# Kernel tuning notes

Hardware: AMD Instinct MI355X
Metric: run time of the kernel (lower is better)

## Reference

```python
import jax, jax.numpy as jnp
import numpy as np

B, N, E, H = 4, 2048, 512, 8
D = E // H  # head dim = 64


def setup_inputs() -> dict:
    key = jax.random.key(0)
    ks = jax.random.split(key, 5)
    s = 1.0 / np.sqrt(E)
    return {
        "x": jax.random.normal(ks[0], (B, N, E), dtype=jnp.float32),
        "Wk": jax.random.normal(ks[1], (E, E), dtype=jnp.float32) * s,
        "bk": jax.random.normal(ks[2], (E,), dtype=jnp.float32) * s,
        "Wv": jax.random.normal(ks[3], (E, E), dtype=jnp.float32) * s,
        "bv": jax.random.normal(ks[4], (E,), dtype=jnp.float32) * s,
    }


def reference(x, Wk, bk, Wv, bv):
    b, n, e = x.shape
    # Linear projections (torch Linear: y = x @ W.T + b), split into heads.
    keys = (x @ Wk.T + bk).reshape(b, n, H, D).transpose(0, 2, 1, 3)    # b h n d
    values = (x @ Wv.T + bv).reshape(b, n, H, D).transpose(0, 2, 1, 3)  # b h n d
    # Q = K self-attention: scores [b, h, n, n]
    dotprod = jnp.einsum('bhnd,bhmd->bhnm', keys, keys)
    # softmax over last axis, then unusual POST-softmax scaling by sqrt(emb)
    att = jax.nn.softmax(dotprod, axis=-1) / jnp.sqrt(jnp.asarray(e, x.dtype))
    # dropout p=0 -> identity
    out = jnp.einsum('bhnm,bhmd->bhnd', att, values)
    return out.transpose(0, 2, 1, 3).reshape(b, n, e)
```

## Files before the change

kernel.cpp:

```cpp
#include <hip/hip_runtime.h>

typedef __bf16 bf16_t;
typedef bf16_t bf16x8 __attribute__((ext_vector_type(8)));
typedef float f32x4 __attribute__((ext_vector_type(4)));
typedef short s16x4 __attribute__((ext_vector_type(4)));

#define NSEQ 2048
#define EMB 512
#define HEADS 8
#define HD 64
#define BATCH 4
#define LOG2E 1.4426950408889634f

#define MFMA16(a, b, c) __builtin_amdgcn_mfma_f32_16x16x32_bf16(a, b, c, 0, 0, 0)
#define MFMA1K(a, b, c) __builtin_amdgcn_mfma_f32_16x16x16bf16_1k(a, b, c, 0, 0, 0)


__global__ __launch_bounds__(256, 2) void proj_kernel(
    const float* __restrict__ x,
    const float* __restrict__ Wk, const float* __restrict__ bk,
    const float* __restrict__ Wv, const float* __restrict__ bv,
    bf16_t* __restrict__ Kf, bf16_t* __restrict__ Vf)
{
  __shared__ union {
    struct {
      __align__(16) bf16_t A[2][128][40];
      __align__(16) bf16_t B[2][128][40];
    } s;
    __align__(16) bf16_t T[128][136];
  } u;

  const int t    = threadIdx.x;
  const int w    = t >> 6;
  const int lane = t & 63;
  const int quad = lane >> 4;
  const int l15  = lane & 15;
  const int wr   = w >> 1, wc = w & 1;
  const int m0   = blockIdx.x * 128;
  const int n0   = blockIdx.y * 128;
  const int zz   = (blockIdx.y >= 4);
  const float* __restrict__ W = zz ? Wv : Wk;
  const int nW = n0 - zz * 512;

  const int sr = t >> 3;
  const int sj = t & 7;
  const int sb = sj >> 2, sc = (sj & 3) * 8;

  float4 pa[4][2], pb[4][2];
  auto prefetch = [&](int k0) {
#pragma unroll
    for (int i = 0; i < 4; ++i) {
      const float* xa = x + (size_t)(m0 + sr + i * 32) * EMB + k0 + sj * 8;
      const float* wa = W + (size_t)(nW + sr + i * 32) * EMB + k0 + sj * 8;
      pa[i][0] = *(const float4*)xa; pa[i][1] = *(const float4*)(xa + 4);
      pb[i][0] = *(const float4*)wa; pb[i][1] = *(const float4*)(wa + 4);
    }
  };
  auto pack8 = [](float4 a, float4 b) -> bf16x8 {
    bf16x8 v;
    v[0] = (bf16_t)a.x; v[1] = (bf16_t)a.y; v[2] = (bf16_t)a.z; v[3] = (bf16_t)a.w;
    v[4] = (bf16_t)b.x; v[5] = (bf16_t)b.y; v[6] = (bf16_t)b.z; v[7] = (bf16_t)b.w;
    return v;
  };

  f32x4 acc[4][4] = {};
  prefetch(0);

  for (int it = 0; it < 8; ++it) {
    __syncthreads();
#pragma unroll
    for (int i = 0; i < 4; ++i) {
      *(bf16x8*)(&u.s.A[sb][sr + i * 32][sc]) = pack8(pa[i][0], pa[i][1]);
      *(bf16x8*)(&u.s.B[sb][sr + i * 32][sc]) = pack8(pb[i][0], pb[i][1]);
    }
    __syncthreads();
    if (it < 7) prefetch((it + 1) * 64);

    bf16x8 af[4][2], bf[4][2];
#pragma unroll
    for (int mt = 0; mt < 4; ++mt)
#pragma unroll
      for (int kk = 0; kk < 2; ++kk)
        af[mt][kk] = *(const bf16x8*)(&u.s.A[kk][wr * 64 + mt * 16 + l15][quad * 8]);
#pragma unroll
    for (int nt = 0; nt < 4; ++nt)
#pragma unroll
      for (int kk = 0; kk < 2; ++kk)
        bf[nt][kk] = *(const bf16x8*)(&u.s.B[kk][wc * 64 + nt * 16 + l15][quad * 8]);
#pragma unroll
    for (int kk = 0; kk < 2; ++kk)
#pragma unroll
      for (int mt = 0; mt < 4; ++mt)
#pragma unroll
        for (int nt = 0; nt < 4; ++nt)
          acc[mt][nt] = MFMA16(af[mt][kk], bf[nt][kk], acc[mt][nt]);
  }

  __syncthreads();

#pragma unroll
  for (int mt = 0; mt < 4; ++mt) {
#pragma unroll
    for (int nt = 0; nt < 4; ++nt) {
      const int F = wc * 64 + nt * 16 + l15;
      const int c = n0 + F;
      const float bb = zz ? bv[c - 512] : bk[c];
#pragma unroll
      for (int reg = 0; reg < 4; ++reg) {
        const int R = wr * 64 + mt * 16 + quad * 4 + reg;
        const float v = acc[mt][nt][reg] + bb;
        if (!zz) u.T[R][F] = (bf16_t)v;
        else     u.T[F][R] = (bf16_t)v;
      }
    }
  }
  __syncthreads();

  if (!zz) {
#pragma unroll
    for (int i = 0; i < 8; ++i) {
      const int fi  = i * 4 + w;
      const int hL  = fi >> 4, kk = (fi >> 3) & 1, ktl = fi & 7;
      const bf16x8 v = *(const bf16x8*)(&u.T[ktl * 16 + l15][hL * 64 + kk * 32 + quad * 8]);
      const int gr = m0 + ktl * 16 + l15;
      const int b = gr >> 11, n = gr & (NSEQ - 1);
      const int bh = b * HEADS + (n0 >> 6) + hL;
      bf16_t* dst = Kf + (((size_t)(bh * 128 + (n >> 4)) * 2 + kk)) * 512 + lane * 8;
      *(bf16x8*)dst = v;
    }
  } else {
#pragma unroll
    for (int i = 0; i < 8; ++i) {
      const int fi   = i * 4 + w;
      const int hL   = fi >> 4, dt = (fi >> 2) & 3, k32l = fi & 3;
      const int F = hL * 64 + dt * 16 + l15;
      union { bf16_t h[8]; bf16x8 v; } pk2;
#pragma unroll
      for (int jt = 0; jt < 2; ++jt)
        *(uint2*)(&pk2.h[jt * 4]) =
            *(const uint2*)(&u.T[F][k32l * 32 + jt * 16 + quad * 4]);
      const int gr = m0 + k32l * 32;
      const int b = gr >> 11, n = gr & (NSEQ - 1);
      const int bh = b * HEADS + ((n0 - 512) >> 6) + hL;
      bf16_t* dst = Vf + (((size_t)(bh * 64 + (n >> 5)) * 4 + dt)) * 512 + lane * 8;
      *(bf16x8*)dst = pk2.v;
    }
  }
}

__global__ __launch_bounds__(256, 2) void flash_kernel(
    const bf16_t* __restrict__ Kf, const bf16_t* __restrict__ Vf,
    float* __restrict__ out)
{
  __shared__ struct {
    __align__(16) float Cb[2][4096];
    __align__(16) float Lb[2][64][4];
  } u;

  const int t    = threadIdx.x;
  const int w    = t >> 6;
  const int lane = t & 63;
  const int quad = lane >> 4;
  const int l15  = lane & 15;
  const int rh   = w & 1;
  const int kh   = w >> 1;

  const int bh = blockIdx.x;
  const int b  = bh >> 3, h = bh & 7;
  const int rowbase = blockIdx.y * 128 + rh * 64;
  const int qtile   = rowbase >> 4;

  const bf16_t* __restrict__ Kb = Kf + (size_t)bh * 128 * 2 * 512;
  const bf16_t* __restrict__ Vb = Vf + (size_t)bh * 64 * 4 * 512;

  bf16x8 qf[4][2];
#pragma unroll
  for (int nt = 0; nt < 4; ++nt)
#pragma unroll
    for (int kk = 0; kk < 2; ++kk)
      qf[nt][kk] = *(const bf16x8*)(Kb + ((size_t)(qtile + nt) * 2 + kk) * 512 + lane * 8);

  float mlog[4];
#pragma unroll
  for (int nt = 0; nt < 4; ++nt) {
    float ss = 0.f;
#pragma unroll
    for (int kk = 0; kk < 2; ++kk)
#pragma unroll
      for (int j = 0; j < 8; ++j) {
        const float qv = (float)qf[nt][kk][j];
        ss = fmaf(qv, qv, ss);
      }
    ss += __shfl_xor(ss, 16, 64);
    ss += __shfl_xor(ss, 32, 64);
    mlog[nt] = ss * LOG2E;
  }

  f32x4 accot[4][4] = {};
  float lsum[4] = {0.f, 0.f, 0.f, 0.f};

  auto load_k = [&](int kt, bf16x8 (&dst)[2][2]) {
    const int kb = kt * 4 + kh * 2;
#pragma unroll
    for (int jt = 0; jt < 2; ++jt)
#pragma unroll
      for (int kk = 0; kk < 2; ++kk)
        dst[jt][kk] =
            *(const bf16x8*)(Kb + ((size_t)(kb + jt) * 2 + kk) * 512 + lane * 8);
  };

  auto body = [&](int kt, bf16x8 (&kcur)[2][2], bf16x8 (&knxt)[2][2]) {
    union { bf16x8 v8; s16x4 s4[2]; } vf[4];
    const int v32 = kt * 2 + kh;
#pragma unroll
    for (int dt = 0; dt < 4; ++dt)
      vf[dt].v8 = *(const bf16x8*)(Vb + ((size_t)v32 * 4 + dt) * 512 + lane * 8);

    f32x4 st[2][4] = {};
#pragma unroll
    for (int kk = 0; kk < 2; ++kk)
#pragma unroll
      for (int jt = 0; jt < 2; ++jt)
#pragma unroll
        for (int nt = 0; nt < 4; ++nt)
          st[jt][nt] = MFMA16(kcur[jt][kk], qf[nt][kk], st[jt][nt]);

    load_k(kt + 1 < NSEQ / 64 ? kt + 1 : kt, knxt);

    s16x4 pw[2][4];
#pragma unroll
    for (int jt = 0; jt < 2; ++jt)
#pragma unroll
      for (int nt = 0; nt < 4; ++nt) {
        union { bf16_t h[4]; s16x4 s; } pp;
#pragma unroll
        for (int reg = 0; reg < 4; ++reg) {
          const float p =
              __builtin_amdgcn_exp2f(fmaf(st[jt][nt][reg], LOG2E, -mlog[nt]));
          lsum[nt] += p;
          pp.h[reg] = (bf16_t)p;
        }
        pw[jt][nt] = pp.s;
      }

#pragma unroll
    for (int jt = 0; jt < 2; ++jt)
#pragma unroll
      for (int dt = 0; dt < 4; ++dt)
#pragma unroll
        for (int nt = 0; nt < 4; ++nt)
          accot[dt][nt] = MFMA1K(vf[dt].s4[jt], pw[jt][nt], accot[dt][nt]);
  };

  bf16x8 kA[2][2], kB[2][2];
  load_k(0, kA);
  for (int kt = 0; kt < NSEQ / 64; kt += 2) {
    body(kt,     kA, kB);
    body(kt + 1, kB, kA);
  }

  __syncthreads();
  if (kh == 1) {
#pragma unroll
    for (int dt = 0; dt < 4; ++dt)
#pragma unroll
      for (int nt = 0; nt < 4; ++nt)
        *(f32x4*)(&u.Cb[rh][((dt * 4 + nt) * 64 + lane) * 4]) = accot[dt][nt];
#pragma unroll
    for (int nt = 0; nt < 4; ++nt) u.Lb[rh][lane][nt] = lsum[nt];
  }
  __syncthreads();
  if (kh == 0) {
#pragma unroll
    for (int dt = 0; dt < 4; ++dt)
#pragma unroll
      for (int nt = 0; nt < 4; ++nt)
        accot[dt][nt] += *(const f32x4*)(&u.Cb[rh][((dt * 4 + nt) * 64 + lane) * 4]);

    const float SCL = 0.044194173824159216f;
    float f[4];
#pragma unroll
    for (int nt = 0; nt < 4; ++nt) {
      float l = lsum[nt] + u.Lb[rh][lane][nt];
      l += __shfl_xor(l, 16, 64);
      l += __shfl_xor(l, 32, 64);
      f[nt] = SCL / l;
    }

#pragma unroll
    for (int nt = 0; nt < 4; ++nt) {
      const int n = rowbase + nt * 16 + l15;
      float* op = out + ((size_t)(b * NSEQ + n)) * EMB + h * HD;
#pragma unroll
      for (int dt = 0; dt < 4; ++dt) {
        f32x4 v = accot[dt][nt];
#pragma unroll
        for (int reg = 0; reg < 4; ++reg) v[reg] *= f[nt];
        *(f32x4*)(op + dt * 16 + quad * 4) = v;
      }
    }
  }
}

extern "C" void kernel_launch(void* const* d_in, const int* in_sizes, int n_in,
                              void* d_out, int out_size, void* d_ws, size_t ws_size,
                              hipStream_t stream) {
  const float* x  = (const float*)d_in[0];
  const float* Wk = (const float*)d_in[1];
  const float* bk = (const float*)d_in[2];
  const float* Wv = (const float*)d_in[3];
  const float* bv = (const float*)d_in[4];
  float* out = (float*)d_out;

  bf16_t* Kf = (bf16_t*)d_ws;
  bf16_t* Vf = Kf + (size_t)BATCH * HEADS * NSEQ * HD;

  dim3 pg(8192 / 128, 1024 / 128);
  proj_kernel<<<pg, 256, 0, stream>>>(x, Wk, bk, Wv, bv, Kf, Vf);

  dim3 fg(BATCH * HEADS, NSEQ / 128);
  flash_kernel<<<fg, 256, 0, stream>>>(Kf, Vf, out);
}
```

Measured before the change: 132.9 us.

## Split key sequence four ways per block and halve query rows per block

Each flash block now handles 64 query rows, and its four waves each take a quarter of the key range, where before two row halves each split keys two ways. The grid doubles to 1024 blocks and launch bounds rise to four blocks per SM, aiming for more parallelism and better latency hiding on the many-CU GPU. In exchange, each K/V tile is reused by fewer query rows, so global/L2 traffic rises, and the final reduction now takes a two-stage LDS tree with extra barriers. The tighter launch bound may also force register spills.

New measurement: 399.7 us. 201% more time.

```diff
diff --git a/kernel.cpp b/kernel.cpp
--- a/kernel.cpp
+++ b/kernel.cpp
@@ -148,7 +148,7 @@
   }
 }
 
-__global__ __launch_bounds__(256, 2) void flash_kernel(
+__global__ __launch_bounds__(256, 4) void flash_kernel(
     const bf16_t* __restrict__ Kf, const bf16_t* __restrict__ Vf,
     float* __restrict__ out)
 {
@@ -162,12 +162,11 @@
   const int lane = t & 63;
   const int quad = lane >> 4;
   const int l15  = lane & 15;
-  const int rh   = w & 1;
-  const int kh   = w >> 1;
+  const int kh   = w;
 
   const int bh = blockIdx.x;
   const int b  = bh >> 3, h = bh & 7;
-  const int rowbase = blockIdx.y * 128 + rh * 64;
+  const int rowbase = blockIdx.y * 64;
   const int qtile   = rowbase >> 4;
 
   const bf16_t* __restrict__ Kb = Kf + (size_t)bh * 128 * 2 * 512;
@@ -200,7 +199,7 @@
   float lsum[4] = {0.f, 0.f, 0.f, 0.f};
 
   auto load_k = [&](int kt, bf16x8 (&dst)[2][2]) {
-    const int kb = kt * 4 + kh * 2;
+    const int kb = kt * 8 + kh * 2;
 #pragma unroll
     for (int jt = 0; jt < 2; ++jt)
 #pragma unroll
@@ -211,7 +210,7 @@
 
   auto body = [&](int kt, bf16x8 (&kcur)[2][2], bf16x8 (&knxt)[2][2]) {
     union { bf16x8 v8; s16x4 s4[2]; } vf[4];
-    const int v32 = kt * 2 + kh;
+    const int v32 = kt * 4 + kh;
 #pragma unroll
     for (int dt = 0; dt < 4; ++dt)
       vf[dt].v8 = *(const bf16x8*)(Vb + ((size_t)v32 * 4 + dt) * 512 + lane * 8);
@@ -225,7 +224,7 @@
         for (int nt = 0; nt < 4; ++nt)
           st[jt][nt] = MFMA16(kcur[jt][kk], qf[nt][kk], st[jt][nt]);
 
-    load_k(kt + 1 < NSEQ / 64 ? kt + 1 : kt, knxt);
+    load_k(kt + 1 < 16 ? kt + 1 : kt, knxt);
 
     s16x4 pw[2][4];
 #pragma unroll
@@ -254,34 +253,56 @@
 
   bf16x8 kA[2][2], kB[2][2];
   load_k(0, kA);
-  for (int kt = 0; kt < NSEQ / 64; kt += 2) {
+#pragma unroll 1
+  for (int kt = 0; kt < 16; kt += 2) {
     body(kt,     kA, kB);
     body(kt + 1, kB, kA);
   }
 
   __syncthreads();
-  if (kh == 1) {
+  if (w >= 2) {
+    const int s = w - 2;
 #pragma unroll
     for (int dt = 0; dt < 4; ++dt)
 #pragma unroll
       for (int nt = 0; nt < 4; ++nt)
-        *(f32x4*)(&u.Cb[rh][((dt * 4 + nt) * 64 + lane) * 4]) = accot[dt][nt];
-#pragma unroll
-    for (int nt = 0; nt < 4; ++nt) u.Lb[rh][lane][nt] = lsum[nt];
-  }
-  __syncthreads();
-  if (kh == 0) {
+        *(f32x4*)(&u.Cb[s][((dt * 4 + nt) * 64 + lane) * 4]) = accot[dt][nt];
+#pragma unroll
+    for (int nt = 0; nt < 4; ++nt) u.Lb[s][lane][nt] = lsum[nt];
+  }
+  __syncthreads();
+  if (w < 2) {
 #pragma unroll
     for (int dt = 0; dt < 4; ++dt)
 #pragma unroll
       for (int nt = 0; nt < 4; ++nt)
-        accot[dt][nt] += *(const f32x4*)(&u.Cb[rh][((dt * 4 + nt) * 64 + lane) * 4]);
+        accot[dt][nt] += *(const f32x4*)(&u.Cb[w][((dt * 4 + nt) * 64 + lane) * 4]);
+#pragma unroll
+    for (int nt = 0; nt < 4; ++nt) lsum[nt] += u.Lb[w][lane][nt];
+  }
+  __syncthreads();
+  if (w == 1) {
+#pragma unroll
+    for (int dt = 0; dt < 4; ++dt)
+#pragma unroll
+      for (int nt = 0; nt < 4; ++nt)
+        *(f32x4*)(&u.Cb[0][((dt * 4 + nt) * 64 + lane) * 4]) = accot[dt][nt];
+#pragma unroll
+    for (int nt = 0; nt < 4; ++nt) u.Lb[0][lane][nt] = lsum[nt];
+  }
+  __syncthreads();
+  if (w == 0) {
+#pragma unroll
+    for (int dt = 0; dt < 4; ++dt)
+#pragma unroll
+      for (int nt = 0; nt < 4; ++nt)
+        accot[dt][nt] += *(const f32x4*)(&u.Cb[0][((dt * 4 + nt) * 64 + lane) * 4]);
 
     const float SCL = 0.044194173824159216f;
     float f[4];
 #pragma unroll
     for (int nt = 0; nt < 4; ++nt) {
-      float l = lsum[nt] + u.Lb[rh][lane][nt];
+      float l = lsum[nt] + u.Lb[0][lane][nt];
       l += __shfl_xor(l, 16, 64);
       l += __shfl_xor(l, 32, 64);
       f[nt] = SCL / l;
@@ -318,6 +339,6 @@
   dim3 pg(8192 / 128, 1024 / 128);
   proj_kernel<<<pg, 256, 0, stream>>>(x, Wk, bk, Wv, bv, Kf, Vf);
 
-  dim3 fg(BATCH * HEADS, NSEQ / 128);
+  dim3 fg(BATCH * HEADS, NSEQ / 64);
   flash_kernel<<<fg, 256, 0, stream>>>(Kf, Vf, out);
 }
```
